# Performance work log

Measured on AMD Instinct MI355X. Metric: run time of the kernel, lower is better.

## Reference

```python
import jax, jax.numpy as jnp
import numpy as np

EMBED_DIM = 1024
NUM_HEADS = 16
MICRO_HEADS = 8
HEAD_DIM = EMBED_DIM // NUM_HEADS
N_BLOCKS = NUM_HEADS // MICRO_HEADS
B, N = 2, 2048


def setup_inputs() -> dict:
    key = jax.random.key(0)
    ks = jax.random.split(key, 9)
    s = 1.0 / np.sqrt(EMBED_DIM)
    return {
        "x": jax.random.normal(ks[0], (B, N, EMBED_DIM), dtype=jnp.float32),
        "Wq": jax.random.uniform(ks[1], (EMBED_DIM, EMBED_DIM), jnp.float32, -s, s),
        "bq": jax.random.uniform(ks[2], (EMBED_DIM,), jnp.float32, -s, s),
        "Wk": jax.random.uniform(ks[3], (EMBED_DIM, EMBED_DIM), jnp.float32, -s, s),
        "bk": jax.random.uniform(ks[4], (EMBED_DIM,), jnp.float32, -s, s),
        "Wv": jax.random.uniform(ks[5], (EMBED_DIM, EMBED_DIM), jnp.float32, -s, s),
        "bv": jax.random.uniform(ks[6], (EMBED_DIM,), jnp.float32, -s, s),
        "Wo": jax.random.uniform(ks[7], (EMBED_DIM, EMBED_DIM), jnp.float32, -s, s),
        "bo": jax.random.uniform(ks[8], (EMBED_DIM,), jnp.float32, -s, s),
    }


def _scramble(t, b, n):
    # Replicates torch's Qh[:, :, hs:he, :].contiguous().view(B*mh, N, dh)
    # which is a raw row-major reshape mixing (N, mh) -> (mh, N) per batch.
    # (B, N, E) -> (B, N, nb, mh, dh) -> (B, nb, N, mh, dh) -> raw reshape -> (B, nb, mh, N, dh)
    t = t.reshape(b, n, N_BLOCKS, MICRO_HEADS, HEAD_DIM)
    t = jnp.transpose(t, (0, 2, 1, 3, 4))
    return t.reshape(b, N_BLOCKS, MICRO_HEADS, n, HEAD_DIM)


def reference(x, Wq, bq, Wk, bk, Wv, bv, Wo, bo):
    b, n, e = x.shape
    scale = HEAD_DIM ** -0.5
    Q = x @ Wq.T + bq
    K = x @ Wk.T + bk
    V = x @ Wv.T + bv
    q = _scramble(Q, b, n)  # (B, nb, mh, N, dh)
    k = _scramble(K, b, n)
    v = _scramble(V, b, n)
    s = jnp.einsum("bgmqd,bgmkd->bgmqk", q, k) * scale  # (B, nb, mh, N, N)
    causal = jnp.tril(jnp.ones((n, n), dtype=bool))
    s = jnp.where(causal, s, -jnp.inf)
    p = jax.nn.softmax(s, axis=-1)
    ctx = jnp.einsum("bgmqk,bgmkd->bgmqd", p, v)  # (B, nb, mh, N, dh)
    # inverse raw reshape: (mh, N, dh) -> (N, mh*dh) per (b, g), then concat blocks
    ctx = ctx.reshape(b, N_BLOCKS, n, MICRO_HEADS * HEAD_DIM)
    ctx = jnp.transpose(ctx, (0, 2, 1, 3)).reshape(b, n, e)
    return ctx @ Wo.T + bo
```

## Files before the change

### kernel.cpp

```cpp
#include <hip/hip_runtime.h>
#include <hip/hip_bf16.h>

typedef unsigned short ushortT;
typedef __attribute__((ext_vector_type(8))) short short8;
typedef __attribute__((ext_vector_type(4))) float floatx4;
typedef __attribute__((ext_vector_type(2))) unsigned int uintx2;

__device__ inline ushortT f2bf(float f) {
    union { float f; unsigned int i; } v; v.f = f;
    unsigned int x = v.i;
    return (ushortT)((x + 0x7fffu + ((x >> 16) & 1u)) >> 16);
}

__device__ inline void gl_lds16(const ushortT* g, ushortT* lds) {
    __builtin_amdgcn_global_load_lds(
        (const __attribute__((address_space(1))) unsigned int*)g,
        (__attribute__((address_space(3))) unsigned int*)lds, 16, 0, 0);
}

__global__ __launch_bounds__(256) void cvt_bf16(
    const float* __restrict__ x,
    const float* __restrict__ Wq, const float* __restrict__ Wk,
    const float* __restrict__ Wv, const float* __restrict__ Wo,
    ushortT* __restrict__ xb, ushortT* __restrict__ Wb)
{
    const unsigned tid = blockIdx.x * 256 + threadIdx.x;
    const size_t e = (size_t)tid * 8;
    const float* src;
    ushortT* dst;
    size_t off;
    if (e < (size_t)(4u << 20)) { src = x; dst = xb; off = e; }
    else {
        const size_t r = e - (size_t)(4u << 20);
        const int wsel = (int)(r >> 20);
        off = r & 0xFFFFFu;
        src = (wsel == 0) ? Wq : (wsel == 1) ? Wk : (wsel == 2) ? Wv : Wo;
        dst = Wb + ((size_t)wsel << 20);
    }
    const float4 f0 = ((const float4*)(src + off))[0];
    const float4 f1 = ((const float4*)(src + off))[1];
    union { __hip_bfloat162 h[4]; uint4 u; } pk;
    pk.h[0] = __float22bfloat162_rn(float2{f0.x, f0.y});
    pk.h[1] = __float22bfloat162_rn(float2{f0.z, f0.w});
    pk.h[2] = __float22bfloat162_rn(float2{f1.x, f1.y});
    pk.h[3] = __float22bfloat162_rn(float2{f1.z, f1.w});
    *(uint4*)(dst + off) = pk.u;
}

__global__ __launch_bounds__(512, 2) void gemm_qkv_8p(
    const ushortT* __restrict__ A, const ushortT* __restrict__ Wst,
    const float* __restrict__ b0, const float* __restrict__ b1, const float* __restrict__ b2,
    ushortT* __restrict__ O0, ushortT* __restrict__ O1, ushortT* __restrict__ VT)
{
    __shared__ __align__(16) ushortT sm[65536];

    const int t = threadIdx.x;
    const int bid = blockIdx.x;
    const int wg = (bid & 7) * 24 + (bid >> 3);
    const int mt = wg / 12;
    const int nt = wg - mt * 12;
    const int m0 = mt * 256;
    const int mat = nt >> 2;
    const int n0 = (nt & 3) * 256;
    const ushortT* W = Wst + ((size_t)mat << 20);
    const float* bias = (mat == 0) ? b0 : (mat == 1) ? b1 : b2;
    ushortT* Out     = (mat == 0) ? O0 : O1;
    const float oscale = (mat == 0) ? 0.18033688f : 1.0f;

    const int w = t >> 6, lane = t & 63;
    const int wm = w >> 2, wn = w & 3;
    const int col16 = lane & 15, quad = lane >> 4;
    const int c7 = col16 & 7;

    const int ko[2] = { ((0 + quad) ^ c7) << 3, ((4 + quad) ^ c7) << 3 };
    const int xbase = (wm * 128 + col16) * 64;
    const int wbase = (wn * 64 + col16) * 64;

    const int trow = t >> 3;
    const int sch = (t & 7) ^ (trow & 7);
    const ushortT* gA[4]; const ushortT* gB[4];
    #pragma unroll
    for (int q = 0; q < 4; q++) {
        gA[q] = A + (size_t)(m0 + q * 64 + trow) * 1024 + sch * 8;
        gB[q] = W + (size_t)(n0 + q * 64 + trow) * 1024 + sch * 8;
    }
    const int dst0 = (w << 6) * 8;

    floatx4 acc[8][4];
    #pragma unroll
    for (int i = 0; i < 8; i++)
        #pragma unroll
        for (int j = 0; j < 4; j++) acc[i][j] = (floatx4)0.0f;

    auto issue8 = [&](const int ab, const int bb) {
        #pragma unroll
        for (int q = 0; q < 4; q++) {
            gl_lds16(gA[q], sm + ab + dst0 + q * 4096);
            gl_lds16(gB[q], sm + bb + dst0 + q * 4096);
            gA[q] += 64; gB[q] += 64;
        }
    };

    auto group = [&](const int ab, const int bb) {
        short8 bw[4];
        #pragma unroll
        for (int ks = 0; ks < 2; ks++) {
            #pragma unroll
            for (int mh = 0; mh < 2; mh++) {
                short8 bx[4];
                if (mh == 0) {
                    #pragma unroll
                    for (int nf = 0; nf < 4; nf++)
                        bw[nf] = *(const short8*)(sm + bb + wbase + nf * 1024 + ko[ks]);
                }
                #pragma unroll
                for (int j = 0; j < 4; j++)
                    bx[j] = *(const short8*)(sm + ab + xbase + (mh * 4 + j) * 1024 + ko[ks]);
                __builtin_amdgcn_s_barrier();
                __builtin_amdgcn_s_setprio(1);
                #pragma unroll
                for (int j = 0; j < 4; j++)
                    #pragma unroll
                    for (int nf = 0; nf < 4; nf++)
                        acc[mh * 4 + j][nf] = __builtin_amdgcn_mfma_f32_16x16x32_bf16(
                            bw[nf], bx[j], acc[mh * 4 + j][nf], 0, 0, 0);
                __builtin_amdgcn_s_setprio(0);
                __builtin_amdgcn_s_barrier();
            }
        }
    };

    issue8(0, 16384);
    issue8(32768, 49152);

    #pragma unroll 1
    for (int it = 0; it < 7; ++it) {
        asm volatile("s_waitcnt vmcnt(8)" ::: "memory");
        __builtin_amdgcn_s_barrier();
        group(0, 16384);
        issue8(0, 16384);
        asm volatile("s_waitcnt vmcnt(8)" ::: "memory");
        __builtin_amdgcn_s_barrier();
        group(32768, 49152);
        issue8(32768, 49152);
    }
    asm volatile("s_waitcnt vmcnt(8)" ::: "memory");
    __builtin_amdgcn_s_barrier();
    group(0, 16384);
    asm volatile("s_waitcnt vmcnt(0)" ::: "memory");
    __builtin_amdgcn_s_barrier();
    group(32768, 49152);

    if (mat != 2) {
        #pragma unroll
        for (int mf = 0; mf < 8; mf++) {
            const int m = m0 + wm * 128 + mf * 16 + col16;
            #pragma unroll
            for (int nf = 0; nf < 4; nf++) {
                const int nb = n0 + wn * 64 + nf * 16 + quad * 4;
                const float4 bv4 = *(const float4*)(bias + nb);
                const float v0 = (acc[mf][nf][0] + bv4.x) * oscale;
                const float v1 = (acc[mf][nf][1] + bv4.y) * oscale;
                const float v2 = (acc[mf][nf][2] + bv4.z) * oscale;
                const float v3 = (acc[mf][nf][3] + bv4.w) * oscale;
                union { __hip_bfloat162 h[2]; unsigned long long u; } pk2;
                pk2.h[0] = __float22bfloat162_rn(float2{v0, v1});
                pk2.h[1] = __float22bfloat162_rn(float2{v2, v3});
                *(unsigned long long*)(Out + (size_t)m * 1024 + nb) = pk2.u;
            }
        }
    } else {
        __syncthreads();
        #pragma unroll
        for (int mf = 0; mf < 8; mf++) {
            const int ml = wm * 128 + mf * 16 + col16;
            const int pib = ml * 4 + wn;
            #pragma unroll
            for (int nf = 0; nf < 4; nf++) {
                const int dbase = nf * 16 + quad * 4;
                const float4 bv4 = *(const float4*)(bias + n0 + wn * 64 + dbase);
                sm[(dbase + 0) * 1024 + pib] = f2bf(acc[mf][nf][0] + bv4.x);
                sm[(dbase + 1) * 1024 + pib] = f2bf(acc[mf][nf][1] + bv4.y);
                sm[(dbase + 2) * 1024 + pib] = f2bf(acc[mf][nf][2] + bv4.z);
                sm[(dbase + 3) * 1024 + pib] = f2bf(acc[mf][nf][3] + bv4.w);
            }
        }
        __syncthreads();
        const int b2 = mt >> 3, mhh = mt & 7, gg = n0 >> 9;
        const int p0 = (n0 & 511) >> 6;
        ushortT* vbase = VT + (size_t)((b2 * 2 + gg) * 8 + mhh) * 131072 + p0;
        #pragma unroll
        for (int v = 0; v < 32; v++) {
            const int e = v * 512 + t;
            const int d = e >> 8;
            const int runml = e & 255;
            const uint2 val = *(const uint2*)(sm + d * 1024 + runml * 4);
            *(uint2*)(vbase + d * 2048 + runml * 8) = val;
        }
    }
}

template <bool OUT_F32, bool N64>
__global__ __launch_bounds__(256) void gemm_lds(
    const ushortT* __restrict__ A, const ushortT* __restrict__ Wst,
    const float* __restrict__ b0, const float* __restrict__ b1, const float* __restrict__ b2,
    void* __restrict__ O0, void* __restrict__ O1, void* __restrict__ O2)
{
    constexpr int NT = N64 ? 64 : 128;
    constexpr int NJ = N64 ? 2 : 4;
    constexpr int WQ = N64 ? 2 : 4;
    __shared__ __align__(16) ushortT As[128 * 64];
    __shared__ __align__(16) ushortT Bs[NT * 64];
    const int t = threadIdx.x;
    const int m0 = blockIdx.y * 128;
    const int n0g = blockIdx.x * NT;
    const int mat = n0g >> 10;
    const int n0 = n0g & 1023;
    const ushortT* W = Wst + ((size_t)mat << 20);
    const float* bias = (mat == 0) ? b0 : (mat == 1) ? b1 : b2;
    void* Out        = (mat == 0) ? O0 : (mat == 1) ? O1 : O2;

    const int w = t >> 6, lane = t & 63;
    const int wm = w >> 1, wn = w & 1;
    const int col16 = lane & 15, quad = lane >> 4;

    floatx4 acc[4][NJ];
    for (int i = 0; i < 4; i++)
        for (int j = 0; j < NJ; j++) acc[i][j] = (floatx4)0.0f;

    const int cid0 = w * (N64 ? 128 : 256) + lane;

    for (int k0 = 0; k0 < 1024; k0 += 64) {
        #pragma unroll
        for (int q = 0; q < 4; q++) {
            const int cid = w * 256 + q * 64 + lane;
            const int row = cid >> 3;
            const int sch = (cid & 7) ^ (row & 7);
            gl_lds16(A + (size_t)(m0 + row) * 1024 + k0 + sch * 8,
                     As + (size_t)(w * 256 + q * 64) * 8);
        }
        #pragma unroll
        for (int q = 0; q < WQ; q++) {
            const int cid = cid0 + q * 64;
            const int row = cid >> 3;
            const int sch = (cid & 7) ^ (row & 7);
            gl_lds16(W + (size_t)(n0 + row) * 1024 + k0 + sch * 8,
                     Bs + (size_t)(w * (N64 ? 128 : 256) + q * 64) * 8);
        }
        __syncthreads();
        #pragma unroll
        for (int ks = 0; ks < 64; ks += 32) {
            const int cbase = (ks >> 3) + quad;
            const int sw = col16 & 7;
            short8 a[4], b[NJ];
            #pragma unroll
            for (int i = 0; i < 4; i++) {
                const int row = wm * 64 + i * 16 + col16;
                a[i] = *(const short8*)(As + row * 64 + ((cbase ^ sw) << 3));
            }
            #pragma unroll
            for (int j = 0; j < NJ; j++) {
                const int row = wn * (NT / 2) + j * 16 + col16;
                b[j] = *(const short8*)(Bs + row * 64 + ((cbase ^ sw) << 3));
            }
            #pragma unroll
            for (int i = 0; i < 4; i++)
                #pragma unroll
                for (int j = 0; j < NJ; j++)
                    acc[i][j] = __builtin_amdgcn_mfma_f32_16x16x32_bf16(b[j], a[i], acc[i][j], 0, 0, 0);
        }
        __syncthreads();
    }

    #pragma unroll
    for (int i = 0; i < 4; i++) {
        const int m = m0 + wm * 64 + i * 16 + col16;
        #pragma unroll
        for (int j = 0; j < NJ; j++) {
            const int nb = n0 + wn * (NT / 2) + j * 16 + quad * 4;
            const float4 bv4 = *(const float4*)(bias + nb);
            const float v0 = acc[i][j][0] + bv4.x;
            const float v1 = acc[i][j][1] + bv4.y;
            const float v2 = acc[i][j][2] + bv4.z;
            const float v3 = acc[i][j][3] + bv4.w;
            if constexpr (OUT_F32) {
                *(float4*)((float*)Out + (size_t)m * 1024 + nb) = float4{v0, v1, v2, v3};
            } else {
                union { __hip_bfloat162 h[2]; unsigned long long u; } pk2;
                pk2.h[0] = __float22bfloat162_rn(float2{v0, v1});
                pk2.h[1] = __float22bfloat162_rn(float2{v2, v3});
                *(unsigned long long*)((ushortT*)Out + (size_t)m * 1024 + nb) = pk2.u;
            }
        }
    }
}

__global__ __launch_bounds__(256) void attn(
    const ushortT* __restrict__ Qb, const ushortT* __restrict__ Kb,
    const ushortT* __restrict__ VT, ushortT* __restrict__ Cb)
{
    __shared__ __align__(16) ushortT lds[16384];

    const int t = threadIdx.x;
    const int bid = blockIdx.x;
    const int xcd = bid & 7;
    const int u = bid >> 3;
    const int s = xcd * 4 + (u & 3);
    const int x5 = u >> 2;
    const int qt = (x5 < 8) ? x5 : (x5 < 16) ? (39 - x5)
                 : (x5 < 24) ? (x5 - 8) : (47 - x5);
    const int bb = s >> 4, g = (s >> 3) & 1, mh = s & 7;

    const int w = t >> 6, lane = t & 63;
    const int col16 = lane & 15, quad = lane >> 4;

    const size_t baseoff = (size_t)bb * 2048 * 1024 + (size_t)g * 512;
    const size_t vtbase  = (size_t)s * 64 * 2048;
    const int i0 = mh * 2048 + qt * 64;
    const int qloc = w * 16 + col16;
    const int c7 = col16 & 7;

    short8 qreg[2];
    {
        const int i = i0 + qloc;
        const ushortT* p = Qb + baseoff + (size_t)(i >> 3) * 1024 + (i & 7) * 64;
        qreg[0] = *(const short8*)(p + quad * 8);
        qreg[1] = *(const short8*)(p + 32 + quad * 8);
    }

    int kbo[2];
    kbo[0] = col16 * 64 + (((0 + quad) ^ c7) << 3);
    kbo[1] = col16 * 64 + (((4 + quad) ^ c7) << 3);

    const int cid0 = w * 128 + lane, cid1 = cid0 + 64;
    const int row0 = cid0 >> 3, sch0 = (cid0 & 7) ^ (row0 & 7);
    const int row1 = cid1 >> 3, sch1 = (cid1 & 7) ^ (row1 & 7);
    const int jr0 = mh * 2048 + row0;
    const int jr1 = mh * 2048 + row1;
    const ushortT* gk0 = Kb + baseoff + (size_t)(jr0 >> 3) * 1024 + (jr0 & 7) * 64 + sch0 * 8;
    const ushortT* gk1 = Kb + baseoff + (size_t)(jr1 >> 3) * 1024 + (jr1 & 7) * 64 + sch1 * 8;
    const ushortT* gv0 = VT + vtbase + (size_t)row0 * 2048 + sch0 * 8;
    const ushortT* gv1 = VT + vtbase + (size_t)row1 * 2048 + sch1 * 8;
    const int sdK = w * 1024;

    auto stage = [&](int sb) {
        gl_lds16(gk0, lds + sb + sdK);
        gl_lds16(gk1, lds + sb + sdK + 512);
        gl_lds16(gv0, lds + sb + 8192 + sdK);
        gl_lds16(gv1, lds + sb + 8192 + sdK + 512);
        gk0 += 8192; gk1 += 8192; gv0 += 64; gv1 += 64;
    };

    float l4[4] = {0.f, 0.f, 0.f, 0.f};
    floatx4 Oacc[4];
    for (int c = 0; c < 4; c++) Oacc[c] = (floatx4)0.0f;

    stage(0);
    int sb = 4096;
    for (int kt = 0; kt <= qt; ++kt) {
        __syncthreads();
        if (kt < qt) { stage(sb); sb ^= 4096; }

        floatx4 sc[4];
        for (int c = 0; c < 4; c++) sc[c] = (floatx4)0.0f;
        #pragma unroll
        for (int h = 0; h < 2; h++) {
            const short8 bq = qreg[h];
            #pragma unroll
            for (int c = 0; c < 4; c++) {
                const short8 ak = *(const short8*)(lds + kbo[h] + c * 1024);
                sc[c] = __builtin_amdgcn_mfma_f32_16x16x32_bf16(ak, bq, sc[c], 0, 0, 0);
            }
        }

        if (kt == qt) {
            #pragma unroll
            for (int c = 0; c < 4; c++)
                #pragma unroll
                for (int r = 0; r < 4; r++)
                    if ((c * 16 + quad * 4 + r) > qloc) sc[c][r] = -1e30f;
        }

        unsigned pw[4][2];
        #pragma unroll
        for (int c = 0; c < 4; c++) {
            float pv0 = __builtin_amdgcn_exp2f(sc[c][0]);
            float pv1 = __builtin_amdgcn_exp2f(sc[c][1]);
            float pv2 = __builtin_amdgcn_exp2f(sc[c][2]);
            float pv3 = __builtin_amdgcn_exp2f(sc[c][3]);
            l4[0] += pv0; l4[1] += pv1; l4[2] += pv2; l4[3] += pv3;
            union { __hip_bfloat162 h; unsigned u; } a, b;
            a.h = __float22bfloat162_rn(float2{pv0, pv1});
            b.h = __float22bfloat162_rn(float2{pv2, pv3});
            pw[c][0] = a.u; pw[c][1] = b.u;
        }

        #pragma unroll
        for (int h = 0; h < 2; h++) {
            unsigned dw[4];
            #pragma unroll
            for (int uu = 0; uu < 2; uu++) {
                uintx2 s32 = __builtin_amdgcn_permlane32_swap(pw[2 * h][uu], pw[2 * h + 1][uu], false, false);
                uintx2 s16 = __builtin_amdgcn_permlane16_swap(s32.x, s32.y, false, false);
                dw[uu] = s16.x; dw[2 + uu] = s16.y;
            }
            union { unsigned u[4]; short8 s; } bpu;
            bpu.u[0] = dw[0]; bpu.u[1] = dw[1]; bpu.u[2] = dw[2]; bpu.u[3] = dw[3];
            const short8 bp = bpu.s;
            #pragma unroll
            for (int c = 0; c < 4; c++) {
                const short8 av = *(const short8*)(lds + kbo[h] + 8192 + c * 1024);
                Oacc[c] = __builtin_amdgcn_mfma_f32_16x16x32_bf16(av, bp, Oacc[c], 0, 0, 0);
            }
        }

        kbo[0] ^= 4096; kbo[1] ^= 4096;
    }

    float l_s = (l4[0] + l4[1]) + (l4[2] + l4[3]);
    l_s += __shfl_xor(l_s, 16);
    l_s += __shfl_xor(l_s, 32);

    {
        const int i = i0 + qloc;
        const float inv = 1.0f / l_s;
        ushortT* dst = Cb + baseoff + (size_t)(i >> 3) * 1024 + (i & 7) * 64;
        #pragma unroll
        for (int c = 0; c < 4; c++) {
            union { __hip_bfloat162 h[2]; unsigned long long u; } pk2;
            pk2.h[0] = __float22bfloat162_rn(float2{Oacc[c][0] * inv, Oacc[c][1] * inv});
            pk2.h[1] = __float22bfloat162_rn(float2{Oacc[c][2] * inv, Oacc[c][3] * inv});
            *(unsigned long long*)(dst + c * 16 + quad * 4) = pk2.u;
        }
    }
}

extern "C" void kernel_launch(void* const* d_in, const int* in_sizes, int n_in,
                              void* d_out, int out_size, void* d_ws, size_t ws_size,
                              hipStream_t stream)
{
    const float* x  = (const float*)d_in[0];
    const float* Wq = (const float*)d_in[1];
    const float* bq = (const float*)d_in[2];
    const float* Wk = (const float*)d_in[3];
    const float* bk = (const float*)d_in[4];
    const float* Wv = (const float*)d_in[5];
    const float* bv = (const float*)d_in[6];
    const float* Wo = (const float*)d_in[7];
    const float* bo = (const float*)d_in[8];

    const size_t M1 = (size_t)1024 * 1024;
    ushortT* Wb  = (ushortT*)d_ws;
    ushortT* xb  = Wb + 4 * M1;
    ushortT* Qb  = xb + 4 * M1;
    ushortT* Kb  = Qb + 4 * M1;
    ushortT* VTb = Wb + 16 * M1;
    ushortT* Cb  = Qb;

    dim3 blk(256);
    cvt_bf16<<<dim3(4096), blk, 0, stream>>>(x, Wq, Wk, Wv, Wo, xb, Wb);
    gemm_qkv_8p<<<dim3(192), dim3(512), 0, stream>>>(
        xb, Wb, bq, bk, bv, Qb, Kb, VTb);
    attn<<<dim3(1024), blk, 0, stream>>>(Qb, Kb, VTb, Cb);
    gemm_lds<true, true><<<dim3(16, 32), blk, 0, stream>>>(
        Cb, Wb + 3 * M1, bo, bo, bo, d_out, d_out, d_out);
}
```

Baseline: 178.5 us.

## Process 128-query tiles per 512-thread attention block sharing K/V staging

The attention kernel now uses 512-thread blocks that each handle 128 query rows (two 64-row sub-tiles) instead of 64, so each staged K/V tile in LDS serves twice as many waves. Each thread issues one K and one V async load per tile instead of two, and the causal mask is generalised to the last two tiles. The grid is halved and the query-tile pairing is remapped for load balance. The aim is to cut global/LDS staging traffic per query; in exchange blocks are coarser and the upper wave's work on the first diagonal tile is fully masked.

After: 177.1 us, median of 2. Within noise of the previous version (-0.8%).

```diff
diff --git a/kernel.cpp b/kernel.cpp
--- a/kernel.cpp
+++ b/kernel.cpp
@@ -295,7 +295,7 @@
     }
 }
 
-__global__ __launch_bounds__(256) void attn(
+__global__ __launch_bounds__(512, 4) void attn(
     const ushortT* __restrict__ Qb, const ushortT* __restrict__ Kb,
     const ushortT* __restrict__ VT, ushortT* __restrict__ Cb)
 {
@@ -306,9 +306,8 @@
     const int xcd = bid & 7;
     const int u = bid >> 3;
     const int s = xcd * 4 + (u & 3);
-    const int x5 = u >> 2;
-    const int qt = (x5 < 8) ? x5 : (x5 < 16) ? (39 - x5)
-                 : (x5 < 24) ? (x5 - 8) : (47 - x5);
+    const int x4 = u >> 2;
+    const int p = (x4 < 8) ? x4 : 23 - x4;
     const int bb = s >> 4, g = (s >> 3) & 1, mh = s & 7;
 
     const int w = t >> 6, lane = t & 63;
@@ -316,39 +315,34 @@
 
     const size_t baseoff = (size_t)bb * 2048 * 1024 + (size_t)g * 512;
     const size_t vtbase  = (size_t)s * 64 * 2048;
-    const int i0 = mh * 2048 + qt * 64;
+    const int i0 = mh * 2048 + p * 128;
+    const int ntile = 2 * p + 2;
     const int qloc = w * 16 + col16;
     const int c7 = col16 & 7;
 
     short8 qreg[2];
     {
         const int i = i0 + qloc;
-        const ushortT* p = Qb + baseoff + (size_t)(i >> 3) * 1024 + (i & 7) * 64;
-        qreg[0] = *(const short8*)(p + quad * 8);
-        qreg[1] = *(const short8*)(p + 32 + quad * 8);
+        const ushortT* ptr = Qb + baseoff + (size_t)(i >> 3) * 1024 + (i & 7) * 64;
+        qreg[0] = *(const short8*)(ptr + quad * 8);
+        qreg[1] = *(const short8*)(ptr + 32 + quad * 8);
     }
 
     int kbo[2];
     kbo[0] = col16 * 64 + (((0 + quad) ^ c7) << 3);
     kbo[1] = col16 * 64 + (((4 + quad) ^ c7) << 3);
 
-    const int cid0 = w * 128 + lane, cid1 = cid0 + 64;
-    const int row0 = cid0 >> 3, sch0 = (cid0 & 7) ^ (row0 & 7);
-    const int row1 = cid1 >> 3, sch1 = (cid1 & 7) ^ (row1 & 7);
-    const int jr0 = mh * 2048 + row0;
-    const int jr1 = mh * 2048 + row1;
-    const ushortT* gk0 = Kb + baseoff + (size_t)(jr0 >> 3) * 1024 + (jr0 & 7) * 64 + sch0 * 8;
-    const ushortT* gk1 = Kb + baseoff + (size_t)(jr1 >> 3) * 1024 + (jr1 & 7) * 64 + sch1 * 8;
-    const ushortT* gv0 = VT + vtbase + (size_t)row0 * 2048 + sch0 * 8;
-    const ushortT* gv1 = VT + vtbase + (size_t)row1 * 2048 + sch1 * 8;
-    const int sdK = w * 1024;
+    const int row = t >> 3;
+    const int sch = (t & 7) ^ (row & 7);
+    const int jr = mh * 2048 + row;
+    const ushortT* gk = Kb + baseoff + (size_t)(jr >> 3) * 1024 + (jr & 7) * 64 + sch * 8;
+    const ushortT* gv = VT + vtbase + (size_t)row * 2048 + sch * 8;
+    const int sdK = w * 512;
 
     auto stage = [&](int sb) {
-        gl_lds16(gk0, lds + sb + sdK);
-        gl_lds16(gk1, lds + sb + sdK + 512);
-        gl_lds16(gv0, lds + sb + 8192 + sdK);
-        gl_lds16(gv1, lds + sb + 8192 + sdK + 512);
-        gk0 += 8192; gk1 += 8192; gv0 += 64; gv1 += 64;
+        gl_lds16(gk, lds + sb + sdK);
+        gl_lds16(gv, lds + sb + 8192 + sdK);
+        gk += 8192; gv += 64;
     };
 
     float l4[4] = {0.f, 0.f, 0.f, 0.f};
@@ -357,9 +351,10 @@
 
     stage(0);
     int sb = 4096;
-    for (int kt = 0; kt <= qt; ++kt) {
+    #pragma unroll 1
+    for (int kt = 0; kt < ntile; ++kt) {
         __syncthreads();
-        if (kt < qt) { stage(sb); sb ^= 4096; }
+        if (kt < ntile - 1) { stage(sb); sb ^= 4096; }
 
         floatx4 sc[4];
         for (int c = 0; c < 4; c++) sc[c] = (floatx4)0.0f;
@@ -373,12 +368,14 @@
             }
         }
 
-        if (kt == qt) {
+        const int dk = kt - 2 * p;
+        if (dk >= 0) {
+            const int qe = qloc - 64 * dk;
             #pragma unroll
             for (int c = 0; c < 4; c++)
                 #pragma unroll
                 for (int r = 0; r < 4; r++)
-                    if ((c * 16 + quad * 4 + r) > qloc) sc[c][r] = -1e30f;
+                    if ((c * 16 + quad * 4 + r) > qe) sc[c][r] = -1e30f;
         }
 
         unsigned pw[4][2];
@@ -404,9 +401,9 @@
                 uintx2 s16 = __builtin_amdgcn_permlane16_swap(s32.x, s32.y, false, false);
                 dw[uu] = s16.x; dw[2 + uu] = s16.y;
             }
-            union { unsigned u[4]; short8 s; } bpu;
-            bpu.u[0] = dw[0]; bpu.u[1] = dw[1]; bpu.u[2] = dw[2]; bpu.u[3] = dw[3];
-            const short8 bp = bpu.s;
+            union { unsigned u2[4]; short8 s2; } bpu;
+            bpu.u2[0] = dw[0]; bpu.u2[1] = dw[1]; bpu.u2[2] = dw[2]; bpu.u2[3] = dw[3];
+            const short8 bp = bpu.s2;
             #pragma unroll
             for (int c = 0; c < 4; c++) {
                 const short8 av = *(const short8*)(lds + kbo[h] + 8192 + c * 1024);
@@ -427,10 +424,10 @@
         ushortT* dst = Cb + baseoff + (size_t)(i >> 3) * 1024 + (i & 7) * 64;
         #pragma unroll
         for (int c = 0; c < 4; c++) {
-            union { __hip_bfloat162 h[2]; unsigned long long u; } pk2;
+            union { __hip_bfloat162 h[2]; unsigned long long u2; } pk2;
             pk2.h[0] = __float22bfloat162_rn(float2{Oacc[c][0] * inv, Oacc[c][1] * inv});
             pk2.h[1] = __float22bfloat162_rn(float2{Oacc[c][2] * inv, Oacc[c][3] * inv});
-            *(unsigned long long*)(dst + c * 16 + quad * 4) = pk2.u;
+            *(unsigned long long*)(dst + c * 16 + quad * 4) = pk2.u2;
         }
     }
 }
@@ -461,7 +458,7 @@
     cvt_bf16<<<dim3(4096), blk, 0, stream>>>(x, Wq, Wk, Wv, Wo, xb, Wb);
     gemm_qkv_8p<<<dim3(192), dim3(512), 0, stream>>>(
         xb, Wb, bq, bk, bv, Qb, Kb, VTb);
-    attn<<<dim3(1024), blk, 0, stream>>>(Qb, Kb, VTb, Cb);
+    attn<<<dim3(512), dim3(512), 0, stream>>>(Qb, Kb, VTb, Cb);
     gemm_lds<true, true><<<dim3(16, 32), blk, 0, stream>>>(
         Cb, Wb + 3 * M1, bo, bo, bo, d_out, d_out, d_out);
 }
```
